# Kernel tuning notes

Measured on AMD Instinct MI355X. Metric: run time of the kernel, lower is better.

## Reference

```python
import jax, jax.numpy as jnp
import numpy as np

B, H, W = 8, 256, 256
GH, GW = 32, 32          # orig_grid_shape, = img / 2^3 after three stride-2 convs
N_STEPS = 6              # masks_num: r_x_total=3, r_y_total=3, alternating dim_stride
C_FEAT = 64
N_MASK = 4               # 4 shifted supervoxel masks summed in setup
DN = ('NHWC', 'HWIO', 'NHWC')
# deconves_importances[r_x-1]; r_x sequence over steps = 1,1,2,2,3,3
LOSS_W = (0.1, 0.1, 0.5, 0.5, 1.0, 1.0)


def _conv(x, w, b, strides=(1, 1)):
    return jax.lax.conv_general_dilated(x, w, strides, 'SAME', dimension_numbers=DN) + b


def _trio(x, w, b, strides=(1, 1)):
    # Conv_trio: conv + channel norm + gelu
    y = _conv(x, w, b, strides)
    mu = jnp.mean(y, axis=-1, keepdims=True)
    var = jnp.var(y, axis=-1, keepdims=True)
    y = (y - mu) * jax.lax.rsqrt(var + 1e-6)
    return jax.nn.gelu(y)


def setup_inputs() -> dict:
    key = jax.random.key(0)
    ks = jax.random.split(key, 8)
    s = 0.05
    w1 = jax.random.normal(ks[0], (3, 3, 1, 16), jnp.float32) * s
    w2 = jax.random.normal(ks[1], (3, 3, 16, 16), jnp.float32) * s
    w3 = jax.random.normal(ks[2], (3, 3, 16, 32), jnp.float32) * s
    w4 = jax.random.normal(ks[3], (3, 3, 32, C_FEAT), jnp.float32) * s
    up_w = jax.random.normal(ks[4], (3, 3, C_FEAT, C_FEAT), jnp.float32) * s
    mask_w = jax.random.normal(ks[5], (3, 3, C_FEAT, N_MASK), jnp.float32) * s
    b1 = jnp.zeros((16,)); b2 = jnp.zeros((16,)); b3 = jnp.zeros((32,))
    b4 = jnp.zeros((C_FEAT,)); up_b = jnp.zeros((C_FEAT,)); mask_b = jnp.zeros((N_MASK,))
    # initial supervoxel masks: sum of 4 shifted checkerboards -> per-cell grid ids
    xs = jnp.arange(GH) % 2
    ys = jnp.arange(GW) % 2
    ids = (xs[:, None] + 2 * ys[None, :]).astype(jnp.float32)  # [GH,GW] in {0,1,2,3}
    masks0 = jnp.broadcast_to(ids[None, :, :, None], (B, GH, GW, 1))
    image = jax.random.normal(ks[6], (B, H, W, 1), jnp.float32)
    return {"image": image, "dynamic_cfg": 0,
            "w1": w1, "b1": b1, "w2": w2, "b2": b2, "w3": w3, "b3": b3,
            "w4": w4, "b4": b4, "up_w": up_w, "up_b": up_b,
            "mask_w": mask_w, "mask_b": mask_b, "masks0": masks0}


def reference(image, dynamic_cfg, w1, b1, w2, b2, w3, b3, w4, b4,
              up_w, up_b, mask_w, mask_b, masks0):
    # encoder: Conv_trio(16) -> (16,s2) -> (32,s2) -> (64,s2)
    x = _trio(image, w1, b1)
    x = _trio(x, w2, b2, (2, 2))
    x = _trio(x, w3, b3, (2, 2))
    deconv_multi = _trio(x, w4, b4, (2, 2))  # [B,32,32,64]
    masks = masks0
    losses = jnp.zeros((1,), image.dtype)
    offsets = jnp.arange(N_MASK, dtype=image.dtype)
    for i in range(N_STEPS):  # fixed, structurally distinct resolutions
        dim = i % 2  # alternating dim_stride as in r_x_r_y_dim_stride
        strides = (2, 1) if dim == 0 else (1, 2)
        deconv_multi = jax.nn.gelu(
            jax.lax.conv_transpose(deconv_multi, up_w, strides, 'SAME',
                                   dimension_numbers=DN) + up_b)
        probs = jax.nn.softmax(_conv(deconv_multi, mask_w, mask_b), axis=-1)  # [B,h,w,4]
        masks = jnp.repeat(masks, 2, axis=dim + 1)
        masks = masks + 0.25 * jnp.sum(probs * offsets, axis=-1, keepdims=True)
        h, w_ = deconv_multi.shape[1], deconv_multi.shape[2]
        img_ds = image.reshape(B, h, H // h, w_, W // w_, 1).mean(axis=(2, 4))
        recon = jnp.sum(probs * offsets, axis=-1, keepdims=True) / 3.0
        entropy = -jnp.sum(probs * jnp.log(probs + 1e-8), axis=-1)
        losses = losses + LOSS_W[i] * (jnp.mean(entropy) + jnp.mean((recon - img_ds) ** 2))
    return losses, masks
```

## Files before the change

### kernel.cpp

```cpp
#include <hip/hip_runtime.h>
#include <hip/hip_bf16.h>
#include <math.h>

typedef __hip_bfloat16 bf16;
typedef float f32x4 __attribute__((ext_vector_type(4)));
typedef __bf16 bf16x8 __attribute__((ext_vector_type(8)));

#define DEV __device__ __forceinline__

DEV float to_f(float v){ return v; }
DEV float to_f(bf16 v){ return __bfloat162float(v); }
DEV bf16 f2b(float v){ return __float2bfloat16(v); }
DEV unsigned short b2u(bf16 v){ return __builtin_bit_cast(unsigned short, v); }

DEV float gelu_f(float x){
  float z = 1.5957691216057308f*(x + 0.044715f*x*x*x);
  float e = __expf(-z);
  return x * __builtin_amdgcn_rcpf(1.0f + e);
}

DEV bf16x8 load_frag(const bf16* p, bool ok){
  uint4 u = make_uint4(0u,0u,0u,0u);
  if (ok) u = *(const uint4*)p;
  return __builtin_bit_cast(bf16x8, u);
// ... 198 lines not shown
}

template<int HI, int WI>
__global__ void upconv_dim0(const bf16* __restrict__ in, const bf16* __restrict__ bpack,
                            const float* __restrict__ upb, bf16* __restrict__ out){
  constexpr int HO = 2*HI, WO = WI, XT = WI/32;
  int lane = threadIdx.x & 63, wv = threadIdx.x >> 6;
  int wtile = swz8(blockIdx.x, gridDim.x)*4 + wv;
  int m = lane & 15, quad = lane >> 4;

  int x0 = (wtile % XT)*32;
  int o  = (wtile / XT) % HO;
  int b  = wtile / (XT*HO);

  int q = o >> 1;
  int stk[2], stq[2]; int nst;
  if (o & 1){ stk[0]=1; stq[0]=q; nst=1; }
  else {
    nst = 0;
    if (q >= 1){ stk[0]=0; stq[0]=q-1; nst=1; }
    stk[nst]=2; stq[nst]=q; nst++;
  }

  f32x4 acc[2][4];
  #pragma unroll
  for (int t=0;t<2;t++)
    #pragma unroll
    for (int nt=0;nt<4;nt++) acc[t][nt] = (f32x4){0.f,0.f,0.f,0.f};

  const uint4* bp4 = (const uint4*)bpack;

  #pragma unroll 1
  for (int s=0; s<nst; s++){
    int kyt = stk[s];
    const bf16* rowp = in + ((size_t)(b*HI+stq[s])*WI)*64 + quad*8;
    #pragma unroll
    for (int ut=0; ut<3; ut++){
      #pragma unroll
      for (int c=0;c<2;c++){
        int ix0 = x0 + m - 1 + ut;
        int ix1 = ix0 + 16;
        bf16x8 a0 = load_frag(rowp + (size_t)ix0*64 + c*32, ix0>=0 && ix0<WI);
        bf16x8 a1 = load_frag(rowp + (size_t)ix1*64 + c*32, ix1>=0 && ix1<WI);
        #pragma unroll
        for (int nt=0;nt<4;nt++){
          uint4 Bq = bp4[(((kyt*3+ut)*2+c)*4+nt)*64 + lane];
          acc[0][nt] = mfma16(a0, Bq, acc[0][nt]);
          acc[1][nt] = mfma16(a1, Bq, acc[1][nt]);
        }
      }
    }
  }

  float4 bv = *(const float4*)(upb + m*4);
  size_t rowbase = ((size_t)b*HO + o)*WO;
  #pragma unroll
  for (int t=0;t<2;t++){
    #pragma unroll
    for (int r=0;r<4;r++){
      int p = x0 + t*16 + quad*4 + r;
      float g0 = gelu_f(acc[t][0][r] + bv.x);
      float g1 = gelu_f(acc[t][1][r] + bv.y);
      float g2 = gelu_f(acc[t][2][r] + bv.z);
      float g3 = gelu_f(acc[t][3][r] + bv.w);
      unsigned int lo = (unsigned int)b2u(f2b(g0)) | ((unsigned int)b2u(f2b(g1))<<16);
      unsigned int hi = (unsigned int)b2u(f2b(g2)) | ((unsigned int)b2u(f2b(g3))<<16);
      *(uint2*)(out + (rowbase + p)*64 + m*4) = make_uint2(lo,hi);
    }
  }
}

template<int HI, int WI>
__global__ void __launch_bounds__(256,2)
upconv_dim0_bs(const bf16* __restrict__ in, const bf16* __restrict__ bpack,
               const float* __restrict__ upb, bf16* __restrict__ out){
  constexpr int HO = 2*HI, WO = WI, XT = WI/32;
  __shared__ __align__(16) uint4 Bsh[4608];
  int tid = threadIdx.x, lane = tid & 63, wv = tid >> 6;
  int wtile = swz8(blockIdx.x, gridDim.x)*4 + wv;
  int m = lane & 15, quad = lane >> 4;

  int x0 = (wtile % XT)*32;
  int o  = (wtile / XT) % HO;
  int b  = wtile / (XT*HO);

  {
    const uint4* gp = (const uint4*)bpack;
    #pragma unroll
    for (int k=0;k<18;k++){
      int base = (wv*18 + k)*64;
      dma16(gp + base + lane, Bsh + base);
    }
  }

  int q = o >> 1;
  int stk[2], stq[2]; int nst;
  if (o & 1){ stk[0]=1; stq[0]=q; nst=1; }
  else {
    nst = 0;
    if (q >= 1){ stk[0]=0; stq[0]=q-1; nst=1; }
    stk[nst]=2; stq[nst]=q; nst++;
  }

  f32x4 acc[2][4];
  #pragma unroll
  for (int t=0;t<2;t++)
    #pragma unroll
    for (int nt=0;nt<4;nt++) acc[t][nt] = (f32x4){0.f,0.f,0.f,0.f};

  asm volatile("s_waitcnt vmcnt(0)" ::: "memory");
  __syncthreads();

  #pragma unroll 1
  for (int s=0; s<nst; s++){
    int kyt = stk[s];
    const bf16* rowp = in + ((size_t)(b*HI+stq[s])*WI)*64 + quad*8;
    #pragma unroll
    for (int ut=0; ut<3; ut++){
      #pragma unroll
      for (int c=0;c<2;c++){
        int ix0 = x0 + m - 1 + ut;
        int ix1 = ix0 + 16;
        bf16x8 a0 = load_frag(rowp + (size_t)ix0*64 + c*32, ix0>=0 && ix0<WI);
        bf16x8 a1 = load_frag(rowp + (size_t)ix1*64 + c*32, ix1>=0 && ix1<WI);
        #pragma unroll
        for (int nt=0;nt<4;nt++){
          uint4 Bq = Bsh[(((kyt*3+ut)*2+c)*4+nt)*64 + lane];
          acc[0][nt] = mfma16(a0, Bq, acc[0][nt]);
          acc[1][nt] = mfma16(a1, Bq, acc[1][nt]);
        }
      }
    }
  }

  float4 bv = *(const float4*)(upb + m*4);
  size_t rowbase = ((size_t)b*HO + o)*WO;
  #pragma unroll
  for (int t=0;t<2;t++){
    #pragma unroll
    for (int r=0;r<4;r++){
      int p = x0 + t*16 + quad*4 + r;
      float g0 = gelu_f(acc[t][0][r] + bv.x);
      float g1 = gelu_f(acc[t][1][r] + bv.y);
      float g2 = gelu_f(acc[t][2][r] + bv.z);
      float g3 = gelu_f(acc[t][3][r] + bv.w);
      unsigned int lo = (unsigned int)b2u(f2b(g0)) | ((unsigned int)b2u(f2b(g1))<<16);
      unsigned int hi = (unsigned int)b2u(f2b(g2)) | ((unsigned int)b2u(f2b(g3))<<16);
      *(uint2*)(out + (rowbase + p)*64 + m*4) = make_uint2(lo,hi);
    }
  }
}

template<int HI, int WI>
__global__ void __launch_bounds__(512,4)
upconv_dim0_bs8(const bf16* __restrict__ in, const bf16* __restrict__ bpack,
                const float* __restrict__ upb, bf16* __restrict__ out){
  constexpr int HO = 2*HI, WO = WI, XT = WI/32;
  __shared__ __align__(16) uint4 Bsh[4608];
  int tid = threadIdx.x, lane = tid & 63, wv = tid >> 6;
  int wtile = swz8(blockIdx.x, gridDim.x)*8 + wv;
  int m = lane & 15, quad = lane >> 4;

  int x0 = (wtile % XT)*32;
  int o  = (wtile / XT) % HO;
  int b  = wtile / (XT*HO);

  {
    const uint4* gp = (const uint4*)bpack;
    #pragma unroll
    for (int k=0;k<9;k++){
      int base = (wv*9 + k)*64;
      dma16(gp + base + lane, Bsh + base);
    }
  }

  int q = o >> 1;
  int stk[2], stq[2]; int nst;
  if (o & 1){ stk[0]=1; stq[0]=q; nst=1; }
  else {
    nst = 0;
    if (q >= 1){ stk[0]=0; stq[0]=q-1; nst=1; }
    stk[nst]=2; stq[nst]=q; nst++;
  }

  f32x4 acc[2][4];
  #pragma unroll
  for (int t=0;t<2;t++)
    #pragma unroll
    for (int nt=0;nt<4;nt++) acc[t][nt] = (f32x4){0.f,0.f,0.f,0.f};

  asm volatile("s_waitcnt vmcnt(0)" ::: "memory");
  __syncthreads();

  #pragma unroll 1
  for (int s=0; s<nst; s++){
    int kyt = stk[s];
    const bf16* rowp = in + ((size_t)(b*HI+stq[s])*WI)*64 + quad*8;
    #pragma unroll
    for (int ut=0; ut<3; ut++){
      #pragma unroll
      for (int c=0;c<2;c++){
        int ix0 = x0 + m - 1 + ut;
        int ix1 = ix0 + 16;
        bf16x8 a0 = load_frag(rowp + (size_t)ix0*64 + c*32, ix0>=0 && ix0<WI);
        bf16x8 a1 = load_frag(rowp + (size_t)ix1*64 + c*32, ix1>=0 && ix1<WI);
        #pragma unroll
        for (int nt=0;nt<4;nt++){
          uint4 Bq = Bsh[(((kyt*3+ut)*2+c)*4+nt)*64 + lane];
          acc[0][nt] = mfma16(a0, Bq, acc[0][nt]);
          acc[1][nt] = mfma16(a1, Bq, acc[1][nt]);
        }
      }
    }
  }

  float4 bv = *(const float4*)(upb + m*4);
  size_t rowbase = ((size_t)b*HO + o)*WO;
  #pragma unroll
  for (int t=0;t<2;t++){
    #pragma unroll
    for (int r=0;r<4;r++){
      int p = x0 + t*16 + quad*4 + r;
      float g0 = gelu_f(acc[t][0][r] + bv.x);
      float g1 = gelu_f(acc[t][1][r] + bv.y);
      float g2 = gelu_f(acc[t][2][r] + bv.z);
      float g3 = gelu_f(acc[t][3][r] + bv.w);
      unsigned int lo = (unsigned int)b2u(f2b(g0)) | ((unsigned int)b2u(f2b(g1))<<16);
      unsigned int hi = (unsigned int)b2u(f2b(g2)) | ((unsigned int)b2u(f2b(g3))<<16);
      *(uint2*)(out + (rowbase + p)*64 + m*4) = make_uint2(lo,hi);
    }
  }
}

template<int HI, int WI>
__global__ void upconv_dim1(const bf16* __restrict__ in, const bf16* __restrict__ bpack,
                            const float* __restrict__ upb, bf16* __restrict__ out){
  constexpr int HO = HI, WO = 2*WI, QT = WI/16;
  int lane = threadIdx.x & 63, wv = threadIdx.x >> 6;
  int wtile = swz8(blockIdx.x, gridDim.x)*4 + wv;
  int m = lane & 15, quad = lane >> 4;

  int q0 = (wtile % QT)*16;
  int y  = (wtile / QT) % HI;
  int b  = wtile / (QT*HI);

  f32x4 ae[4], ao[4];
  #pragma unroll
  for (int nt=0;nt<4;nt++){ ae[nt]=(f32x4){0.f,0.f,0.f,0.f}; ao[nt]=(f32x4){0.f,0.f,0.f,0.f}; }

  const uint4* bp4 = (const uint4*)bpack;

  #pragma unroll 1
  for (int ky=0; ky<3; ky++){
    int iy = y + ky - 1;
    if (iy < 0 || iy >= HI) continue;
    const bf16* rowp = in + ((size_t)(b*HI+iy)*WI)*64 + quad*8;
    #pragma unroll
    for (int c=0;c<2;c++){
      int qa = q0 + m;
      bf16x8 Au = load_frag(rowp + (size_t)qa*64 + c*32, true);
      bf16x8 As = load_frag(rowp + (size_t)(qa-1)*64 + c*32, qa >= 1);
      #pragma unroll
      for (int nt=0;nt<4;nt++){
        uint4 B0 = bp4[(((ky*3+0)*2+c)*4+nt)*64 + lane];
        uint4 B1 = bp4[(((ky*3+1)*2+c)*4+nt)*64 + lane];
        uint4 B2 = bp4[(((ky*3+2)*2+c)*4+nt)*64 + lane];
        ae[nt] = mfma16(As, B0, ae[nt]);
        ae[nt] = mfma16(Au, B2, ae[nt]);
        ao[nt] = mfma16(Au, B1, ao[nt]);
      }
    }
  }

  float4 bv = *(const float4*)(upb + m*4);
  size_t rowbase = ((size_t)b*HO + y)*WO;
  #pragma unroll
  for (int r=0;r<4;r++){
    int qq = q0 + quad*4 + r;
    {
      float g0 = gelu_f(ae[0][r] + bv.x);
      float g1 = gelu_f(ae[1][r] + bv.y);
      float g2 = gelu_f(ae[2][r] + bv.z);
      float g3 = gelu_f(ae[3][r] + bv.w);
      unsigned int lo = (unsigned int)b2u(f2b(g0)) | ((unsigned int)b2u(f2b(g1))<<16);
      unsigned int hi = (unsigned int)b2u(f2b(g2)) | ((unsigned int)b2u(f2b(g3))<<16);
      *(uint2*)(out + (rowbase + 2*qq)*64 + m*4) = make_uint2(lo,hi);
    }
    {
      float g0 = gelu_f(ao[0][r] + bv.x);
      float g1 = gelu_f(ao[1][r] + bv.y);
      float g2 = gelu_f(ao[2][r] + bv.z);
      float g3 = gelu_f(ao[3][r] + bv.w);
      unsigned int lo = (unsigned int)b2u(f2b(g0)) | ((unsigned int)b2u(f2b(g1))<<16);
      unsigned int hi = (unsigned int)b2u(f2b(g2)) | ((unsigned int)b2u(f2b(g3))<<16);
      *(uint2*)(out + (rowbase + 2*qq+1)*64 + m*4) = make_uint2(lo,hi);
    }
  }
}

template<int HI, int WI>
__global__ void __launch_bounds__(256,2)
upconv_dim1_bs(const bf16* __restrict__ in, const bf16* __restrict__ bpack,
               const float* __restrict__ upb, bf16* __restrict__ out){
  constexpr int HO = HI, WO = 2*WI, QT = WI/16;
  __shared__ __align__(16) uint4 Bsh[4608];
  int tid = threadIdx.x, lane = tid & 63, wv = tid >> 6;
  int wtile = swz8(blockIdx.x, gridDim.x)*4 + wv;
  int m = lane & 15, quad = lane >> 4;

  int q0 = (wtile % QT)*16;
  int y  = ((wtile / QT) % (HI/2)) * 2;
  int b  = wtile / (QT*(HI/2));

  {
    const uint4* gp = (const uint4*)bpack;
    #pragma unroll
    for (int k=0;k<18;k++){
      int base = (wv*18 + k)*64;
      dma16(gp + base + lane, Bsh + base);
    }
  }

  int qa = q0 + m;

  bf16x8 Afr[4][2][2];
  #pragma unroll
  for (int i4=0;i4<4;i4++){
    int iy = y + i4 - 1;
    bool ok = (iy>=0) && (iy<HI);
    const bf16* rowp = in + ((size_t)(b*HI+iy)*WI)*64 + quad*8;
    #pragma unroll
    for (int c=0;c<2;c++){
      Afr[i4][c][0] = load_frag(rowp + (size_t)qa*64 + c*32, ok);
      Afr[i4][c][1] = load_frag(rowp + (size_t)(qa-1)*64 + c*32, ok && qa >= 1);
    }
  }

  asm volatile("s_waitcnt vmcnt(0)" ::: "memory");
  __syncthreads();

  f32x4 ae[2][4], ao[2][4];
  #pragma unroll
  for (int r=0;r<2;r++)
    #pragma unroll
    for (int nt=0;nt<4;nt++){ ae[r][nt]=(f32x4){0.f,0.f,0.f,0.f}; ao[r][nt]=(f32x4){0.f,0.f,0.f,0.f}; }

  #pragma unroll
  for (int ky=0; ky<3; ky++){
    #pragma unroll
    for (int c=0;c<2;c++){
      #pragma unroll
      for (int nt=0;nt<4;nt++){
        uint4 B0 = Bsh[(((ky*3+0)*2+c)*4+nt)*64 + lane];
        uint4 B1 = Bsh[(((ky*3+1)*2+c)*4+nt)*64 + lane];
        uint4 B2 = Bsh[(((ky*3+2)*2+c)*4+nt)*64 + lane];
        #pragma unroll
        for (int r=0;r<2;r++){
          ae[r][nt] = mfma16(Afr[ky+r][c][1], B0, ae[r][nt]);
          ae[r][nt] = mfma16(Afr[ky+r][c][0], B2, ae[r][nt]);
          ao[r][nt] = mfma16(Afr[ky+r][c][0], B1, ao[r][nt]);
        }
      }
    }
  }

  float4 bv = *(const float4*)(upb + m*4);
  #pragma unroll
  for (int r2=0;r2<2;r2++){
    size_t rowbase = ((size_t)b*HO + y + r2)*WO;
    #pragma unroll
    for (int r=0;r<4;r++){
      int qq = q0 + quad*4 + r;
      {
        float g0 = gelu_f(ae[r2][0][r] + bv.x);
        float g1 = gelu_f(ae[r2][1][r] + bv.y);
        float g2 = gelu_f(ae[r2][2][r] + bv.z);
        float g3 = gelu_f(ae[r2][3][r] + bv.w);
        unsigned int lo = (unsigned int)b2u(f2b(g0)) | ((unsigned int)b2u(f2b(g1))<<16);
        unsigned int hi = (unsigned int)b2u(f2b(g2)) | ((unsigned int)b2u(f2b(g3))<<16);
        *(uint2*)(out + (rowbase + 2*qq)*64 + m*4) = make_uint2(lo,hi);
      }
      {
        float g0 = gelu_f(ao[r2][0][r] + bv.x);
        float g1 = gelu_f(ao[r2][1][r] + bv.y);
        float g2 = gelu_f(ao[r2][2][r] + bv.z);
        float g3 = gelu_f(ao[r2][3][r] + bv.w);
        unsigned int lo = (unsigned int)b2u(f2b(g0)) | ((unsigned int)b2u(f2b(g1))<<16);
        unsigned int hi = (unsigned int)b2u(f2b(g2)) | ((unsigned int)b2u(f2b(g3))<<16);
        *(uint2*)(out + (rowbase + 2*qq+1)*64 + m*4) = make_uint2(lo,hi);
      }
    }
  }
}

template<int HI, int WI>
__global__ void __launch_bounds__(512,4)
upconv_dim1_bs8(const bf16* __restrict__ in, const bf16* __restrict__ bpack,
                const float* __restrict__ upb, bf16* __restrict__ out){
  constexpr int HO = HI, WO = 2*WI, QT = WI/16;
  __shared__ __align__(16) uint4 Bsh[4608];
  int tid = threadIdx.x, lane = tid & 63, wv = tid >> 6;
  int wtile = swz8(blockIdx.x, gridDim.x)*8 + wv;
  int m = lane & 15, quad = lane >> 4;

  int q0 = (wtile % QT)*16;
  int y  = ((wtile / QT) % (HI/2)) * 2;
  int b  = wtile / (QT*(HI/2));

  {
    const uint4* gp = (const uint4*)bpack;
    #pragma unroll
    for (int k=0;k<9;k++){
      int base = (wv*9 + k)*64;
      dma16(gp + base + lane, Bsh + base);
    }
  }

  int qa = q0 + m;

  bf16x8 Afr[4][2][2];
  #pragma unroll
  for (int i4=0;i4<4;i4++){
    int iy = y + i4 - 1;
    bool ok = (iy>=0) && (iy<HI);
    const bf16* rowp = in + ((size_t)(b*HI+iy)*WI)*64 + quad*8;
    #pragma unroll
    for (int c=0;c<2;c++){
      Afr[i4][c][0] = load_frag(rowp + (size_t)qa*64 + c*32, ok);
      Afr[i4][c][1] = load_frag(rowp + (size_t)(qa-1)*64 + c*32, ok && qa >= 1);
    }
  }

  asm volatile("s_waitcnt vmcnt(0)" ::: "memory");
  __syncthreads();

  f32x4 ae[2][4], ao[2][4];
  #pragma unroll
  for (int r=0;r<2;r++)
    #pragma unroll
    for (int nt=0;nt<4;nt++){ ae[r][nt]=(f32x4){0.f,0.f,0.f,0.f}; ao[r][nt]=(f32x4){0.f,0.f,0.f,0.f}; }

  #pragma unroll
  for (int ky=0; ky<3; ky++){
    #pragma unroll
    for (int c=0;c<2;c++){
      #pragma unroll
      for (int nt=0;nt<4;nt++){
        uint4 B0 = Bsh[(((ky*3+0)*2+c)*4+nt)*64 + lane];
        uint4 B1 = Bsh[(((ky*3+1)*2+c)*4+nt)*64 + lane];
        uint4 B2 = Bsh[(((ky*3+2)*2+c)*4+nt)*64 + lane];
        #pragma unroll
        for (int r=0;r<2;r++){
          ae[r][nt] = mfma16(Afr[ky+r][c][1], B0, ae[r][nt]);
          ae[r][nt] = mfma16(Afr[ky+r][c][0], B2, ae[r][nt]);
          ao[r][nt] = mfma16(Afr[ky+r][c][0], B1, ao[r][nt]);
        }
      }
    }
  }

  float4 bv = *(const float4*)(upb + m*4);
  #pragma unroll
  for (int r2=0;r2<2;r2++){
    size_t rowbase = ((size_t)b*HO + y + r2)*WO;
    #pragma unroll
    for (int r=0;r<4;r++){
      int qq = q0 + quad*4 + r;
      {
        float g0 = gelu_f(ae[r2][0][r] + bv.x);
        float g1 = gelu_f(ae[r2][1][r] + bv.y);
        float g2 = gelu_f(ae[r2][2][r] + bv.z);
        float g3 = gelu_f(ae[r2][3][r] + bv.w);
        unsigned int lo = (unsigned int)b2u(f2b(g0)) | ((unsigned int)b2u(f2b(g1))<<16);
        unsigned int hi = (unsigned int)b2u(f2b(g2)) | ((unsigned int)b2u(f2b(g3))<<16);
        *(uint2*)(out + (rowbase + 2*qq)*64 + m*4) = make_uint2(lo,hi);
      }
      {
        float g0 = gelu_f(ao[r2][0][r] + bv.x);
        float g1 = gelu_f(ao[r2][1][r] + bv.y);
        float g2 = gelu_f(ao[r2][2][r] + bv.z);
        float g3 = gelu_f(ao[r2][3][r] + bv.w);
        unsigned int lo = (unsigned int)b2u(f2b(g0)) | ((unsigned int)b2u(f2b(g1))<<16);
        unsigned int hi = (unsigned int)b2u(f2b(g2)) | ((unsigned int)b2u(f2b(g3))<<16);
        *(uint2*)(out + (rowbase + 2*qq+1)*64 + m*4) = make_uint2(lo,hi);
      }
    }
  }
}

template<int STEP, int DIM, int HH, int WW, int TILES>
__global__ void maskloss_mfma(const bf16* __restrict__ feat, const bf16* __restrict__ mpack,
                              const float* __restrict__ mb, const float* __restrict__ img,
                              const float* __restrict__ masks_in, float* __restrict__ masks_out,
                              float* __restrict__ accbuf){
  __shared__ float llog[4][64][4];
  __shared__ float red[4][2];
  int lane = threadIdx.x & 63;
  int wv   = threadIdx.x >> 6;
  int wtile = swz8(blockIdx.x, gridDim.x)*4 + wv;
  int m = lane & 15, quad = lane >> 4;

  constexpr int TPR = WW/(16*TILES);
  int x0 = (wtile % TPR)*(16*TILES);
  int y  = (wtile / TPR) % HH;
  int b  = wtile / (TPR*HH);

  const uint4* bp4 = (const uint4*)mpack;

  #pragma unroll 1
  for (int t=0; t<TILES; t++){
    f32x4 acc4 = (f32x4){0.f,0.f,0.f,0.f};
    #pragma unroll
    for (int c=0;c<2;c++){
      bf16x8 afr[9];
      #pragma unroll
      for (int ky=0; ky<3; ky++){
        int iy = y + ky - 1;
        bool rowok = (iy >= 0) && (iy < HH);
        const bf16* rowp = feat + ((size_t)(b*HH+iy)*WW)*64 + quad*8 + c*32;
        #pragma unroll
        for (int kx=0; kx<3; kx++){
          int ix = x0 + t*16 + m + kx - 1;
          bool ok = rowok && (ix >= 0) && (ix < WW);
          afr[ky*3+kx] = load_frag(rowp + (size_t)ix*64, ok);
        }
      }
      #pragma unroll
      for (int tap=0; tap<9; tap++){
        uint4 bb = bp4[(tap*2+c)*64 + lane];
        acc4 = mfma16(afr[tap], bb, acc4);
      }
    }
    if (m < 4){
      #pragma unroll
      for (int r=0;r<4;r++) llog[wv][t*16 + quad*4 + r][m] = acc4[r] + mb[m];
    }
  }
  __syncthreads();

  float ent = 0.f, mse = 0.f;
  if (lane < 16*TILES){
    int p = lane; int xx = x0 + p;
    float l0 = llog[wv][p][0], l1 = llog[wv][p][1];
    float l2 = llog[wv][p][2], l3 = llog[wv][p][3];
    float mx = fmaxf(fmaxf(l0,l1), fmaxf(l2,l3));
    float d0=l0-mx, d1=l1-mx, d2=l2-mx, d3=l3-mx;
    float e0=__expf(d0), e1=__expf(d1), e2=__expf(d2), e3=__expf(d3);
    float S = e0+e1+e2+e3;
    float inv = __builtin_amdgcn_rcpf(S);
    float sval = (e1 + 2.f*e2 + 3.f*e3)*inv;

    constexpr int HM = (DIM==0)? HH/2 : HH;
    constexpr int WM = (DIM==0)? WW : WW/2;
    int my = (DIM==0)? (y>>1) : y;
    int mxi = (DIM==1)? (xx>>1) : xx;
    float mv = masks_in[((size_t)b*HM + my)*WM + mxi];
    masks_out[((size_t)b*HH + y)*WW + xx] = mv + 0.25f*sval;

    ent = __logf(S) - (e0*d0 + e1*d1 + e2*d2 + e3*d3)*inv;

    constexpr int FH = 256/HH, FW = 256/WW;
    float isum = 0.f;
    const float* ib = img + ((size_t)b*256 + y*FH)*256 + xx*FW;
    #pragma unroll
    for (int dy=0; dy<FH; dy++)
      #pragma unroll
// ... 118 lines not shown
    constexpr int FH = 256/HH, FW = 256/WW;
    float isum = 0.f;
    const float* ib = img + ((size_t)b*256 + yw*FH)*256 + xx*FW;
    #pragma unroll
    for (int dy=0; dy<FH; dy++)
      #pragma unroll
      for (int dx=0; dx<FW; dx++) isum += ib[dy*256+dx];
    float img_ds = isum * (1.0f/(FH*FW));
    float d = sval*(1.0f/3.0f) - img_ds;
    mse = d*d;
  }

  #pragma unroll
  for (int off=1; off<64; off<<=1){
    ent += __shfl_xor(ent, off, 64);
    mse += __shfl_xor(mse, off, 64);
  }
  if (lane == 0){ red[wv][0] = ent; red[wv][1] = mse; }
  __syncthreads();
  if (threadIdx.x == 0){
    float e  = red[0][0] + red[1][0] + red[2][0] + red[3][0];
    float ms = red[0][1] + red[1][1] + red[2][1] + red[3][1];
    int slot = blockIdx.x & (NSLOT-1);
    atomicAdd(accbuf + (2*STEP  )*NSLOT + slot, e);
    atomicAdd(accbuf + (2*STEP+1)*NSLOT + slot, ms);
  }
}

template<int STEP, int DIM, int HH, int WW>
__global__ void __launch_bounds__(512,4)
maskloss_lds8(const bf16* __restrict__ feat, const bf16* __restrict__ mpack,
              const float* __restrict__ mb, const float* __restrict__ img,
              const float* __restrict__ masks_in, float* __restrict__ masks_out,
              float* __restrict__ accbuf){
  constexpr int NBrow = WW/64;
  constexpr int PITCH = 9216;
  constexpr int NR = 6;
  __shared__ __align__(16) char smem[NR*PITCH];
  __shared__ float llog[8][2][16][4];
  __shared__ float red[8][2];
  int tid = threadIdx.x;
  int lane = tid & 63, wv = tid >> 6;
  int bi = swz8(blockIdx.x, gridDim.x);
  int x0 = (bi % NBrow)*64;
  int y0 = ((bi / NBrow) % (HH/4)) * 4;
  int b  = bi / (NBrow*(HH/4));
  int m = lane & 15, quad = lane >> 4;
  int lanesw = ((lane ^ (lane>>3)) << 4);

  int r_w   = wv >> 1;
  int xbase = (wv & 1) * 32;
  int yw    = y0 + r_w;

  for (int k = wv; k < NR*9; k += 8){
    int r = k/9, coff = (k%9)*1024;
    int iy = y0 + r - 1;
    if (iy < 0 || iy >= HH) continue;
    const char* g = (const char*)(feat + ((size_t)(b*HH+iy)*WW + x0 - 1)*64)
                    + coff + lanesw;
    dma16(g, smem + r*PITCH + coff);
  }
  asm volatile("s_waitcnt vmcnt(0)" ::: "memory");
  __syncthreads();
  if (x0 == 0 && tid < 32*NR)
    ((float*)(smem + (tid>>5)*PITCH))[tid & 31] = 0.f;
  if (x0 + 64 == WW && tid >= 256 && tid < 256 + 32*NR){
    int t = tid - 256;
    ((float*)(smem + (t>>5)*PITCH + 65*128))[t & 31] = 0.f;
  }
  __syncthreads();

  const uint4* bp4 = (const uint4*)mpack;
  #pragma unroll
  for (int t=0; t<2; t++){
    f32x4 accA = (f32x4){0.f,0.f,0.f,0.f};
    f32x4 accB = (f32x4){0.f,0.f,0.f,0.f};
    #pragma unroll
    for (int ky=0; ky<3; ky++){
      int iyw = yw + ky - 1;
      if (iyw < 0 || iyw >= HH) continue;
      const char* rowl = smem + (size_t)(r_w + ky)*PITCH;
      #pragma unroll
      for (int kx=0; kx<3; kx++){
        int lp = xbase + t*16 + m + kx;
        const char* pl = rowl + (size_t)lp*128;
        int xw = (lp & 7) << 4;
        bf16x8 a0 = __builtin_bit_cast(bf16x8, *(const uint4*)(pl + ((quad*16     ) ^ xw)));
        bf16x8 a1 = __builtin_bit_cast(bf16x8, *(const uint4*)(pl + ((quad*16 + 64) ^ xw)));
        uint4 b0 = bp4[((ky*3+kx)*2+0)*64 + lane];
        uint4 b1 = bp4[((ky*3+kx)*2+1)*64 + lane];
        accA = mfma16(a0, b0, accA);
        accB = mfma16(a1, b1, accB);
      }
    }
    if (m < 4){
      #pragma unroll
      for (int r=0;r<4;r++) llog[wv][t][quad*4+r][m] = accA[r] + accB[r] + mb[m];
    }
  }
  __syncthreads();

  float ent = 0.f, mse = 0.f;
  if (lane < 32){
    int t = lane >> 4;
    int p = lane & 15;
    int xx = x0 + xbase + t*16 + p;
    float l0 = llog[wv][t][p][0], l1 = llog[wv][t][p][1];
    float l2 = llog[wv][t][p][2], l3 = llog[wv][t][p][3];
    float mx = fmaxf(fmaxf(l0,l1), fmaxf(l2,l3));
    float d0=l0-mx, d1=l1-mx, d2=l2-mx, d3=l3-mx;
    float e0=__expf(d0), e1=__expf(d1), e2=__expf(d2), e3=__expf(d3);
    float S = e0+e1+e2+e3;
    float inv = __builtin_amdgcn_rcpf(S);
    float sval = (e1 + 2.f*e2 + 3.f*e3)*inv;

    constexpr int HM = (DIM==0)? HH/2 : HH;
    constexpr int WM = (DIM==0)? WW : WW/2;
    int my = (DIM==0)? (yw>>1) : yw;
    int mxi = (DIM==1)? (xx>>1) : xx;
    float mv = masks_in[((size_t)b*HM + my)*WM + mxi];
    masks_out[((size_t)b*HH + yw)*WW + xx] = mv + 0.25f*sval;

    ent = __logf(S) - (e0*d0 + e1*d1 + e2*d2 + e3*d3)*inv;

    constexpr int FH = 256/HH, FW = 256/WW;
    float isum = 0.f;
    const float* ib = img + ((size_t)b*256 + yw*FH)*256 + xx*FW;
    #pragma unroll
    for (int dy=0; dy<FH; dy++)
      #pragma unroll
      for (int dx=0; dx<FW; dx++) isum += ib[dy*256+dx];
    float img_ds = isum * (1.0f/(FH*FW));
    float d = sval*(1.0f/3.0f) - img_ds;
    mse = d*d;
  }

  #pragma unroll
  for (int off=1; off<64; off<<=1){
    ent += __shfl_xor(ent, off, 64);
    mse += __shfl_xor(mse, off, 64);
  }
  if (lane == 0){ red[wv][0] = ent; red[wv][1] = mse; }
  __syncthreads();
  if (threadIdx.x == 0){
    float e = 0.f, ms = 0.f;
    #pragma unroll
    for (int i=0;i<8;i++){ e += red[i][0]; ms += red[i][1]; }
    int slot = blockIdx.x & (NSLOT-1);
    atomicAdd(accbuf + (2*STEP  )*NSLOT + slot, e);
    atomicAdd(accbuf + (2*STEP+1)*NSLOT + slot, ms);
  }
}

__global__ void finalize_kernel(const float* __restrict__ acc, float* __restrict__ out){
  int lane = threadIdx.x & 63;
  float v[12];
  #pragma unroll
  for (int i=0;i<12;i++){
    float x = acc[i*NSLOT + lane];
    #pragma unroll
    for (int off=1; off<64; off<<=1) x += __shfl_xor(x, off, 64);
    v[i] = x;
  }
  if (lane == 0){
    const float lw[6] = {0.1f,0.1f,0.5f,0.5f,1.0f,1.0f};
    const float nn[6] = {16384.f,32768.f,65536.f,131072.f,262144.f,524288.f};
    float L=0.f;
    for (int i=0;i<6;i++) L += lw[i]*((v[2*i] + v[2*i+1])/nn[i]);
    out[0]=L;
  }
}

extern "C" void kernel_launch(void* const* d_in, const int* in_sizes, int n_in,
                              void* d_out, int out_size, void* d_ws, size_t ws_size,
                              hipStream_t stream){
  const float* image  = (const float*)d_in[0];
  const float* w1=(const float*)d_in[2];  const float* b1=(const float*)d_in[3];
  const float* w2=(const float*)d_in[4];  const float* b2=(const float*)d_in[5];
  const float* w3=(const float*)d_in[6];  const float* b3=(const float*)d_in[7];
  const float* w4=(const float*)d_in[8];  const float* b4=(const float*)d_in[9];
  const float* upw=(const float*)d_in[10];const float* upb=(const float*)d_in[11];
  const float* mw=(const float*)d_in[12]; const float* mb=(const float*)d_in[13];
  const float* masks0=(const float*)d_in[14];
  float* out = (float*)d_out;

  char* ws = (char*)d_ws;
  size_t off = 0;
  auto alloc = [&](size_t bytes)->char*{
    char* p = ws + off; off += (bytes + 255) & ~(size_t)255; return p;
  };
  bf16* enc1  = (bf16*)alloc((size_t)8*256*256*16*2);
  bf16* enc2  = (bf16*)alloc((size_t)8*128*128*16*2);
  bf16* enc3  = (bf16*)alloc((size_t)8*64*64*32*2);
  bf16* featA = (bf16*)alloc((size_t)8*256*256*64*2);
  bf16* featB = (bf16*)alloc((size_t)8*256*128*64*2);
  float* mbA  = (float*)alloc((size_t)8*256*128*4);
  float* mbB  = (float*)alloc((size_t)8*128*128*4);
  bf16* packU = (bf16*)alloc((size_t)9*2*4*64*8*2);
  bf16* packM = (bf16*)alloc((size_t)9*2*64*8*2);
  bf16* packT2= (bf16*)alloc((size_t)5*1*64*8*2);
  bf16* packT3= (bf16*)alloc((size_t)5*2*64*8*2);
  bf16* packT4= (bf16*)alloc((size_t)9*4*64*8*2);
  float* acc  = (float*)alloc(12*NSLOT*sizeof(float));

  hipMemsetAsync(acc, 0, 12*NSLOT*sizeof(float), stream);

  repack_all<<<282,256,0,stream>>>(upw, mw, w2, w3, w4,
                                   packU, packM, packT2, packT3, packT4);

  trio_kernel<float,1,16,1,1,256,256><<<8*256*256/256,256,0,stream>>>(image,w1,b1,enc1);
  trio_mfma<16,16,256,256><<<8*128*128/16/4,256,0,stream>>>(enc1,packT2,b2,enc2);
  trio_mfma<16,32,128,128><<<8*64*64/16/4,256,0,stream>>>(enc2,packT3,b3,enc3);
  trio_mfma<32,64,64,64><<<8*32*32/16/4,256,0,stream>>>(enc3,packT4,b4,featA);

  upconv_dim0<32,32><<<128,256,0,stream>>>(featA,packU,upb,featB);
  maskloss_mfma<0,0,64,32,2><<<128,256,0,stream>>>(featB,packM,mb,image,masks0,mbA,acc);
  upconv_dim1<64,32><<<256,256,0,stream>>>(featB,packU,upb,featA);
  maskloss_lds<1,1,64,64,1><<<512,256,0,stream>>>(featA,packM,mb,image,mbA,mbB,acc);
  upconv_dim0_bs<64,64><<<512,256,0,stream>>>(featA,packU,upb,featB);
  maskloss_lds<2,0,128,64,1><<<1024,256,0,stream>>>(featB,packM,mb,image,mbB,mbA,acc);
  upconv_dim1_bs<128,64><<<512,256,0,stream>>>(featB,packU,upb,featA);
  maskloss_lds<3,1,128,128,2><<<1024,256,0,stream>>>(featA,packM,mb,image,mbA,mbB,acc);
  upconv_dim0_bs8<128,128><<<1024,512,0,stream>>>(featA,packU,upb,featB);
  maskloss_lds8<4,0,256,128><<<1024,512,0,stream>>>(featB,packM,mb,image,mbB,mbA,acc);
  upconv_dim1_bs8<256,128><<<1024,512,0,stream>>>(featB,packU,upb,featA);
  maskloss_lds8<5,1,256,256><<<2048,512,0,stream>>>(featA,packM,mb,image,mbA,out+1,acc);

  finalize_kernel<<<1,64,0,stream>>>(acc,out);
}
```

Before: 328.8 us.

## Co-schedule mask-loss and next upconv in one heterogeneous launch

Merges each step's mask/loss kernel with the following upsampling transposed-conv kernel into a single launch. Block indices are split between the two roles in an interleaved pattern, and each role reads the same input feature map. Both roles can do so because the mask branch and the next upconv depend only on the current features. This removes two kernel launches and the serialization between them, letting the two workloads overlap on the device. The cost is a larger shared-memory allocation per block, which may lower occupancy, plus divergent block roles in one kernel.

```diff
diff --git a/kernel.cpp b/kernel.cpp
--- a/kernel.cpp
+++ b/kernel.cpp
@@ -374,87 +374,6 @@
 }
 
 template<int HI, int WI>
-__global__ void __launch_bounds__(512,4)
-upconv_dim0_bs8(const bf16* __restrict__ in, const bf16* __restrict__ bpack,
-                const float* __restrict__ upb, bf16* __restrict__ out){
-  constexpr int HO = 2*HI, WO = WI, XT = WI/32;
-  __shared__ __align__(16) uint4 Bsh[4608];
-  int tid = threadIdx.x, lane = tid & 63, wv = tid >> 6;
-  int wtile = swz8(blockIdx.x, gridDim.x)*8 + wv;
-  int m = lane & 15, quad = lane >> 4;
-
-  int x0 = (wtile % XT)*32;
-  int o  = (wtile / XT) % HO;
-  int b  = wtile / (XT*HO);
-
-  {
-    const uint4* gp = (const uint4*)bpack;
-    #pragma unroll
-    for (int k=0;k<9;k++){
-      int base = (wv*9 + k)*64;
-      dma16(gp + base + lane, Bsh + base);
-    }
-  }
-
-  int q = o >> 1;
-  int stk[2], stq[2]; int nst;
-  if (o & 1){ stk[0]=1; stq[0]=q; nst=1; }
-  else {
-    nst = 0;
-    if (q >= 1){ stk[0]=0; stq[0]=q-1; nst=1; }
-    stk[nst]=2; stq[nst]=q; nst++;
-  }
-
-  f32x4 acc[2][4];
-  #pragma unroll
-  for (int t=0;t<2;t++)
-    #pragma unroll
-    for (int nt=0;nt<4;nt++) acc[t][nt] = (f32x4){0.f,0.f,0.f,0.f};
-
-  asm volatile("s_waitcnt vmcnt(0)" ::: "memory");
-  __syncthreads();
-
-  #pragma unroll 1
-  for (int s=0; s<nst; s++){
-    int kyt = stk[s];
-    const bf16* rowp = in + ((size_t)(b*HI+stq[s])*WI)*64 + quad*8;
-    #pragma unroll
-    for (int ut=0; ut<3; ut++){
-      #pragma unroll
-      for (int c=0;c<2;c++){
-        int ix0 = x0 + m - 1 + ut;
-        int ix1 = ix0 + 16;
-        bf16x8 a0 = load_frag(rowp + (size_t)ix0*64 + c*32, ix0>=0 && ix0<WI);
-        bf16x8 a1 = load_frag(rowp + (size_t)ix1*64 + c*32, ix1>=0 && ix1<WI);
-        #pragma unroll
-        for (int nt=0;nt<4;nt++){
-          uint4 Bq = Bsh[(((kyt*3+ut)*2+c)*4+nt)*64 + lane];
-          acc[0][nt] = mfma16(a0, Bq, acc[0][nt]);
-          acc[1][nt] = mfma16(a1, Bq, acc[1][nt]);
-        }
-      }
-    }
-  }
-
-  float4 bv = *(const float4*)(upb + m*4);
-  size_t rowbase = ((size_t)b*HO + o)*WO;
-  #pragma unroll
-  for (int t=0;t<2;t++){
-    #pragma unroll
-    for (int r=0;r<4;r++){
-      int p = x0 + t*16 + quad*4 + r;
-      float g0 = gelu_f(acc[t][0][r] + bv.x);
-      float g1 = gelu_f(acc[t][1][r] + bv.y);
-      float g2 = gelu_f(acc[t][2][r] + bv.z);
-      float g3 = gelu_f(acc[t][3][r] + bv.w);
-      unsigned int lo = (unsigned int)b2u(f2b(g0)) | ((unsigned int)b2u(f2b(g1))<<16);
-      unsigned int hi = (unsigned int)b2u(f2b(g2)) | ((unsigned int)b2u(f2b(g3))<<16);
-      *(uint2*)(out + (rowbase + p)*64 + m*4) = make_uint2(lo,hi);
-    }
-  }
-}
-
-template<int HI, int WI>
 __global__ void upconv_dim1(const bf16* __restrict__ in, const bf16* __restrict__ bpack,
                             const float* __restrict__ upb, bf16* __restrict__ out){
   constexpr int HO = HI, WO = 2*WI, QT = WI/16;
@@ -539,101 +458,6 @@
     #pragma unroll
     for (int k=0;k<18;k++){
       int base = (wv*18 + k)*64;
-      dma16(gp + base + lane, Bsh + base);
-    }
-  }
-
-  int qa = q0 + m;
-
-  bf16x8 Afr[4][2][2];
-  #pragma unroll
-  for (int i4=0;i4<4;i4++){
-    int iy = y + i4 - 1;
-    bool ok = (iy>=0) && (iy<HI);
-    const bf16* rowp = in + ((size_t)(b*HI+iy)*WI)*64 + quad*8;
-    #pragma unroll
-    for (int c=0;c<2;c++){
-      Afr[i4][c][0] = load_frag(rowp + (size_t)qa*64 + c*32, ok);
-      Afr[i4][c][1] = load_frag(rowp + (size_t)(qa-1)*64 + c*32, ok && qa >= 1);
-    }
-  }
-
-  asm volatile("s_waitcnt vmcnt(0)" ::: "memory");
-  __syncthreads();
-
-  f32x4 ae[2][4], ao[2][4];
-  #pragma unroll
-  for (int r=0;r<2;r++)
-    #pragma unroll
-    for (int nt=0;nt<4;nt++){ ae[r][nt]=(f32x4){0.f,0.f,0.f,0.f}; ao[r][nt]=(f32x4){0.f,0.f,0.f,0.f}; }
-
-  #pragma unroll
-  for (int ky=0; ky<3; ky++){
-    #pragma unroll
-    for (int c=0;c<2;c++){
-      #pragma unroll
-      for (int nt=0;nt<4;nt++){
-        uint4 B0 = Bsh[(((ky*3+0)*2+c)*4+nt)*64 + lane];
-        uint4 B1 = Bsh[(((ky*3+1)*2+c)*4+nt)*64 + lane];
-        uint4 B2 = Bsh[(((ky*3+2)*2+c)*4+nt)*64 + lane];
-        #pragma unroll
-        for (int r=0;r<2;r++){
-          ae[r][nt] = mfma16(Afr[ky+r][c][1], B0, ae[r][nt]);
-          ae[r][nt] = mfma16(Afr[ky+r][c][0], B2, ae[r][nt]);
-          ao[r][nt] = mfma16(Afr[ky+r][c][0], B1, ao[r][nt]);
-        }
-      }
-    }
-  }
-
-  float4 bv = *(const float4*)(upb + m*4);
-  #pragma unroll
-  for (int r2=0;r2<2;r2++){
-    size_t rowbase = ((size_t)b*HO + y + r2)*WO;
-    #pragma unroll
-    for (int r=0;r<4;r++){
-      int qq = q0 + quad*4 + r;
-      {
-        float g0 = gelu_f(ae[r2][0][r] + bv.x);
-        float g1 = gelu_f(ae[r2][1][r] + bv.y);
-        float g2 = gelu_f(ae[r2][2][r] + bv.z);
-        float g3 = gelu_f(ae[r2][3][r] + bv.w);
-        unsigned int lo = (unsigned int)b2u(f2b(g0)) | ((unsigned int)b2u(f2b(g1))<<16);
-        unsigned int hi = (unsigned int)b2u(f2b(g2)) | ((unsigned int)b2u(f2b(g3))<<16);
-        *(uint2*)(out + (rowbase + 2*qq)*64 + m*4) = make_uint2(lo,hi);
-      }
-      {
-        float g0 = gelu_f(ao[r2][0][r] + bv.x);
-        float g1 = gelu_f(ao[r2][1][r] + bv.y);
-        float g2 = gelu_f(ao[r2][2][r] + bv.z);
-        float g3 = gelu_f(ao[r2][3][r] + bv.w);
-        unsigned int lo = (unsigned int)b2u(f2b(g0)) | ((unsigned int)b2u(f2b(g1))<<16);
-        unsigned int hi = (unsigned int)b2u(f2b(g2)) | ((unsigned int)b2u(f2b(g3))<<16);
-        *(uint2*)(out + (rowbase + 2*qq+1)*64 + m*4) = make_uint2(lo,hi);
-      }
-    }
-  }
-}
-
-template<int HI, int WI>
-__global__ void __launch_bounds__(512,4)
-upconv_dim1_bs8(const bf16* __restrict__ in, const bf16* __restrict__ bpack,
-                const float* __restrict__ upb, bf16* __restrict__ out){
-  constexpr int HO = HI, WO = 2*WI, QT = WI/16;
-  __shared__ __align__(16) uint4 Bsh[4608];
-  int tid = threadIdx.x, lane = tid & 63, wv = tid >> 6;
-  int wtile = swz8(blockIdx.x, gridDim.x)*8 + wv;
-  int m = lane & 15, quad = lane >> 4;
-
-  int q0 = (wtile % QT)*16;
-  int y  = ((wtile / QT) % (HI/2)) * 2;
-  int b  = wtile / (QT*(HI/2));
-
-  {
-    const uint4* gp = (const uint4*)bpack;
-    #pragma unroll
-    for (int k=0;k<9;k++){
-      int base = (wv*9 + k)*64;
       dma16(gp + base + lane, Bsh + base);
     }
   }
@@ -1058,6 +882,296 @@
   }
 }
 
+template<int STEP, int DIM, int HH, int WW,
+         int UPD, int HI, int WI,
+         int NU, int NM, int PAT>
+__global__ void __launch_bounds__(512,4)
+fused_mu(const bf16* __restrict__ feat, const bf16* __restrict__ packU,
+         const float* __restrict__ upb, bf16* __restrict__ outFeat,
+         const bf16* __restrict__ packM, const float* __restrict__ mb,
+         const float* __restrict__ img, const float* __restrict__ masks_in,
+         float* __restrict__ masks_out, float* __restrict__ accbuf){
+  __shared__ __align__(16) char shbuf[73728];
+  int tid = threadIdx.x, lane = tid & 63, wv = tid >> 6;
+  int m = lane & 15, quad = lane >> 4;
+
+  bool isU; int uIdx, mIdx;
+  if constexpr (PAT == 0){
+    isU = !(blockIdx.x & 1); uIdx = blockIdx.x >> 1; mIdx = blockIdx.x >> 1;
+  } else {
+    int r3 = blockIdx.x % 3; isU = (r3 != 2);
+    uIdx = (blockIdx.x/3)*2 + r3; mIdx = blockIdx.x/3;
+  }
+
+  if (isU){
+    uint4* Bsh = (uint4*)shbuf;
+    int wtile = swz8(uIdx, NU)*8 + wv;
+    {
+      const uint4* gp = (const uint4*)packU;
+      #pragma unroll
+      for (int k=0;k<9;k++){
+        int base = (wv*9 + k)*64;
+        dma16(gp + base + lane, Bsh + base);
+      }
+    }
+
+    if constexpr (UPD == 0){
+      constexpr int HO = 2*HI, WO = WI, XT = WI/32;
+      int x0 = (wtile % XT)*32;
+      int o  = (wtile / XT) % HO;
+      int b  = wtile / (XT*HO);
+
+      int q = o >> 1;
+      int stk[2], stq[2]; int nst;
+      if (o & 1){ stk[0]=1; stq[0]=q; nst=1; }
+      else {
+        nst = 0;
+        if (q >= 1){ stk[0]=0; stq[0]=q-1; nst=1; }
+        stk[nst]=2; stq[nst]=q; nst++;
+      }
+
+      f32x4 acc[2][4];
+      #pragma unroll
+      for (int t=0;t<2;t++)
+        #pragma unroll
+        for (int nt=0;nt<4;nt++) acc[t][nt] = (f32x4){0.f,0.f,0.f,0.f};
+
+      asm volatile("s_waitcnt vmcnt(0)" ::: "memory");
+      __syncthreads();
+
+      #pragma unroll 1
+      for (int s=0; s<nst; s++){
+        int kyt = stk[s];
+        const bf16* rowp = feat + ((size_t)(b*HI+stq[s])*WI)*64 + quad*8;
+        #pragma unroll
+        for (int ut=0; ut<3; ut++){
+          #pragma unroll
+          for (int c=0;c<2;c++){
+            int ix0 = x0 + m - 1 + ut;
+            int ix1 = ix0 + 16;
+            bf16x8 a0 = load_frag(rowp + (size_t)ix0*64 + c*32, ix0>=0 && ix0<WI);
+            bf16x8 a1 = load_frag(rowp + (size_t)ix1*64 + c*32, ix1>=0 && ix1<WI);
+            #pragma unroll
+            for (int nt=0;nt<4;nt++){
+              uint4 Bq = Bsh[(((kyt*3+ut)*2+c)*4+nt)*64 + lane];
+              acc[0][nt] = mfma16(a0, Bq, acc[0][nt]);
+              acc[1][nt] = mfma16(a1, Bq, acc[1][nt]);
+            }
+          }
+        }
+      }
+
+      float4 bv = *(const float4*)(upb + m*4);
+      size_t rowbase = ((size_t)b*HO + o)*WO;
+      #pragma unroll
+      for (int t=0;t<2;t++){
+        #pragma unroll
+        for (int r=0;r<4;r++){
+          int p = x0 + t*16 + quad*4 + r;
+          float g0 = gelu_f(acc[t][0][r] + bv.x);
+          float g1 = gelu_f(acc[t][1][r] + bv.y);
+          float g2 = gelu_f(acc[t][2][r] + bv.z);
+          float g3 = gelu_f(acc[t][3][r] + bv.w);
+          unsigned int lo = (unsigned int)b2u(f2b(g0)) | ((unsigned int)b2u(f2b(g1))<<16);
+          unsigned int hi = (unsigned int)b2u(f2b(g2)) | ((unsigned int)b2u(f2b(g3))<<16);
+          *(uint2*)(outFeat + (rowbase + p)*64 + m*4) = make_uint2(lo,hi);
+        }
+      }
+    } else {
+      constexpr int HO = HI, WO = 2*WI, QT = WI/16;
+      int q0 = (wtile % QT)*16;
+      int y  = ((wtile / QT) % (HI/2)) * 2;
+      int b  = wtile / (QT*(HI/2));
+      int qa = q0 + m;
+
+      bf16x8 Afr[4][2][2];
+      #pragma unroll
+      for (int i4=0;i4<4;i4++){
+        int iy = y + i4 - 1;
+        bool ok = (iy>=0) && (iy<HI);
+        const bf16* rowp = feat + ((size_t)(b*HI+iy)*WI)*64 + quad*8;
+        #pragma unroll
+        for (int c=0;c<2;c++){
+          Afr[i4][c][0] = load_frag(rowp + (size_t)qa*64 + c*32, ok);
+          Afr[i4][c][1] = load_frag(rowp + (size_t)(qa-1)*64 + c*32, ok && qa >= 1);
+        }
+      }
+
+      asm volatile("s_waitcnt vmcnt(0)" ::: "memory");
+      __syncthreads();
+
+      f32x4 ae[2][4], ao[2][4];
+      #pragma unroll
+      for (int r=0;r<2;r++)
+        #pragma unroll
+        for (int nt=0;nt<4;nt++){ ae[r][nt]=(f32x4){0.f,0.f,0.f,0.f}; ao[r][nt]=(f32x4){0.f,0.f,0.f,0.f}; }
+
+      #pragma unroll
+      for (int ky=0; ky<3; ky++){
+        #pragma unroll
+        for (int c=0;c<2;c++){
+          #pragma unroll
+          for (int nt=0;nt<4;nt++){
+            uint4 B0 = Bsh[(((ky*3+0)*2+c)*4+nt)*64 + lane];
+            uint4 B1 = Bsh[(((ky*3+1)*2+c)*4+nt)*64 + lane];
+            uint4 B2 = Bsh[(((ky*3+2)*2+c)*4+nt)*64 + lane];
+            #pragma unroll
+            for (int r=0;r<2;r++){
+              ae[r][nt] = mfma16(Afr[ky+r][c][1], B0, ae[r][nt]);
+              ae[r][nt] = mfma16(Afr[ky+r][c][0], B2, ae[r][nt]);
+              ao[r][nt] = mfma16(Afr[ky+r][c][0], B1, ao[r][nt]);
+            }
+          }
+        }
+      }
+
+      float4 bv = *(const float4*)(upb + m*4);
+      #pragma unroll
+      for (int r2=0;r2<2;r2++){
+        size_t rowbase = ((size_t)b*HO + y + r2)*WO;
+        #pragma unroll
+        for (int r=0;r<4;r++){
+          int qq = q0 + quad*4 + r;
+          {
+            float g0 = gelu_f(ae[r2][0][r] + bv.x);
+            float g1 = gelu_f(ae[r2][1][r] + bv.y);
+            float g2 = gelu_f(ae[r2][2][r] + bv.z);
+            float g3 = gelu_f(ae[r2][3][r] + bv.w);
+            unsigned int lo = (unsigned int)b2u(f2b(g0)) | ((unsigned int)b2u(f2b(g1))<<16);
+            unsigned int hi = (unsigned int)b2u(f2b(g2)) | ((unsigned int)b2u(f2b(g3))<<16);
+            *(uint2*)(outFeat + (rowbase + 2*qq)*64 + m*4) = make_uint2(lo,hi);
+          }
+          {
+            float g0 = gelu_f(ao[r2][0][r] + bv.x);
+            float g1 = gelu_f(ao[r2][1][r] + bv.y);
+            float g2 = gelu_f(ao[r2][2][r] + bv.z);
+            float g3 = gelu_f(ao[r2][3][r] + bv.w);
+            unsigned int lo = (unsigned int)b2u(f2b(g0)) | ((unsigned int)b2u(f2b(g1))<<16);
+            unsigned int hi = (unsigned int)b2u(f2b(g2)) | ((unsigned int)b2u(f2b(g3))<<16);
+            *(uint2*)(outFeat + (rowbase + 2*qq+1)*64 + m*4) = make_uint2(lo,hi);
+          }
+        }
+      }
+    }
+  } else {
+    constexpr int NBrow = WW/64;
+    constexpr int PITCH = 9216;
+    constexpr int NR = 6;
+    char* smem = shbuf;
+    float* llogb = (float*)(shbuf + NR*PITCH);
+    float* redb  = (float*)(shbuf + NR*PITCH + 8*2*16*4*4);
+    int bi = swz8(mIdx, NM);
+    int x0 = (bi % NBrow)*64;
+    int y0 = ((bi / NBrow) % (HH/4)) * 4;
+    int b  = bi / (NBrow*(HH/4));
+    int lanesw = ((lane ^ (lane>>3)) << 4);
+
+    int r_w   = wv >> 1;
+    int xbase = (wv & 1) * 32;
+    int yw    = y0 + r_w;
+
+    for (int k = wv; k < NR*9; k += 8){
+      int r = k/9, coff = (k%9)*1024;
+      int iy = y0 + r - 1;
+      if (iy < 0 || iy >= HH) continue;
+      const char* g = (const char*)(feat + ((size_t)(b*HH+iy)*WW + x0 - 1)*64)
+                      + coff + lanesw;
+      dma16(g, smem + r*PITCH + coff);
+    }
+    asm volatile("s_waitcnt vmcnt(0)" ::: "memory");
+    __syncthreads();
+    if (x0 == 0 && tid < 32*NR)
+      ((float*)(smem + (tid>>5)*PITCH))[tid & 31] = 0.f;
+    if (x0 + 64 == WW && tid >= 256 && tid < 256 + 32*NR){
+      int t = tid - 256;
+      ((float*)(smem + (t>>5)*PITCH + 65*128))[t & 31] = 0.f;
+    }
+    __syncthreads();
+
+    const uint4* bp4 = (const uint4*)packM;
+    #pragma unroll
+    for (int t=0; t<2; t++){
+      f32x4 accA = (f32x4){0.f,0.f,0.f,0.f};
+      f32x4 accB = (f32x4){0.f,0.f,0.f,0.f};
+      #pragma unroll
+      for (int ky=0; ky<3; ky++){
+        int iyw = yw + ky - 1;
+        if (iyw < 0 || iyw >= HH) continue;
+        const char* rowl = smem + (size_t)(r_w + ky)*PITCH;
+        #pragma unroll
+        for (int kx=0; kx<3; kx++){
+          int lp = xbase + t*16 + m + kx;
+          const char* pl = rowl + (size_t)lp*128;
+          int xw = (lp & 7) << 4;
+          bf16x8 a0 = __builtin_bit_cast(bf16x8, *(const uint4*)(pl + ((quad*16     ) ^ xw)));
+          bf16x8 a1 = __builtin_bit_cast(bf16x8, *(const uint4*)(pl + ((quad*16 + 64) ^ xw)));
+          uint4 b0 = bp4[((ky*3+kx)*2+0)*64 + lane];
+          uint4 b1 = bp4[((ky*3+kx)*2+1)*64 + lane];
+          accA = mfma16(a0, b0, accA);
+          accB = mfma16(a1, b1, accB);
+        }
+      }
+      if (m < 4){
+        #pragma unroll
+        for (int r=0;r<4;r++)
+          llogb[((wv*2 + t)*16 + quad*4 + r)*4 + m] = accA[r] + accB[r] + mb[m];
+      }
+    }
+    __syncthreads();
+
+    float ent = 0.f, mse = 0.f;
+    if (lane < 32){
+      int t = lane >> 4;
+      int p = lane & 15;
+      int xx = x0 + xbase + t*16 + p;
+      float l0 = llogb[((wv*2+t)*16+p)*4+0], l1 = llogb[((wv*2+t)*16+p)*4+1];
+      float l2 = llogb[((wv*2+t)*16+p)*4+2], l3 = llogb[((wv*2+t)*16+p)*4+3];
+      float mx = fmaxf(fmaxf(l0,l1), fmaxf(l2,l3));
+      float d0=l0-mx, d1=l1-mx, d2=l2-mx, d3=l3-mx;
+      float e0=__expf(d0), e1=__expf(d1), e2=__expf(d2), e3=__expf(d3);
+      float S = e0+e1+e2+e3;
+      float inv = __builtin_amdgcn_rcpf(S);
+      float sval = (e1 + 2.f*e2 + 3.f*e3)*inv;
+
+      constexpr int HM = (DIM==0)? HH/2 : HH;
+      constexpr int WM = (DIM==0)? WW : WW/2;
+      int my = (DIM==0)? (yw>>1) : yw;
+      int mxi = (DIM==1)? (xx>>1) : xx;
+      float mv = masks_in[((size_t)b*HM + my)*WM + mxi];
+      masks_out[((size_t)b*HH + yw)*WW + xx] = mv + 0.25f*sval;
+
+      ent = __logf(S) - (e0*d0 + e1*d1 + e2*d2 + e3*d3)*inv;
+
+      constexpr int FH = 256/HH, FW = 256/WW;
+      float isum = 0.f;
+      const float* ib = img + ((size_t)b*256 + yw*FH)*256 + xx*FW;
+      #pragma unroll
+      for (int dy=0; dy<FH; dy++)
+        #pragma unroll
+        for (int dx=0; dx<FW; dx++) isum += ib[dy*256+dx];
+      float img_ds = isum * (1.0f/(FH*FW));
+      float d = sval*(1.0f/3.0f) - img_ds;
+      mse = d*d;
+    }
+
+    #pragma unroll
+    for (int off=1; off<64; off<<=1){
+      ent += __shfl_xor(ent, off, 64);
+      mse += __shfl_xor(mse, off, 64);
+    }
+    if (lane == 0){ redb[wv*2+0] = ent; redb[wv*2+1] = mse; }
+    __syncthreads();
+    if (tid == 0){
+      float e = 0.f, ms = 0.f;
+      #pragma unroll
+      for (int i=0;i<8;i++){ e += redb[i*2+0]; ms += redb[i*2+1]; }
+      int slot = mIdx & (NSLOT-1);
+      atomicAdd(accbuf + (2*STEP  )*NSLOT + slot, e);
+      atomicAdd(accbuf + (2*STEP+1)*NSLOT + slot, ms);
+    }
+  }
+}
+
 __global__ void finalize_kernel(const float* __restrict__ acc, float* __restrict__ out){
   int lane = threadIdx.x & 63;
   float v[12];
@@ -1126,10 +1240,10 @@
   upconv_dim0_bs<64,64><<<512,256,0,stream>>>(featA,packU,upb,featB);
   maskloss_lds<2,0,128,64,1><<<1024,256,0,stream>>>(featB,packM,mb,image,mbB,mbA,acc);
   upconv_dim1_bs<128,64><<<512,256,0,stream>>>(featB,packU,upb,featA);
-  maskloss_lds<3,1,128,128,2><<<1024,256,0,stream>>>(featA,packM,mb,image,mbA,mbB,acc);
-  upconv_dim0_bs8<128,128><<<1024,512,0,stream>>>(featA,packU,upb,featB);
-  maskloss_lds8<4,0,256,128><<<1024,512,0,stream>>>(featB,packM,mb,image,mbB,mbA,acc);
-  upconv_dim1_bs8<256,128><<<1024,512,0,stream>>>(featB,packU,upb,featA);
+  fused_mu<3,1,128,128, 0,128,128, 1024,512,1>
+      <<<1536,512,0,stream>>>(featA,packU,upb,featB,packM,mb,image,mbA,mbB,acc);
+  fused_mu<4,0,256,128, 1,256,128, 1024,1024,0>
+      <<<2048,512,0,stream>>>(featB,packU,upb,featA,packM,mb,image,mbB,mbA,acc);
   maskloss_lds8<5,1,256,256><<<2048,512,0,stream>>>(featA,packM,mb,image,mbA,out+1,acc);
 
   finalize_kernel<<<1,64,0,stream>>>(acc,out);
```

After: 331.3 us. Within noise of the previous version (+0.7%).
